# Kernel optimization log

Hardware: AMD Instinct MI355X
Metric: run time of the kernel (lower is better)

The kernel has to match this reference:

```python
import jax, jax.numpy as jnp
import numpy as np

STEP = 1  # spatial shift amount (module hard-codes narrow offset 1, so step=1)
EPS = 1e-5  # BatchNorm eps (torch default)


def conv1x1(x, W, b):
    # x: [B,C,H,W], W: [Co,C], b: [Co]
    return jnp.einsum('bchw,oc->bohw', x, W) + b[None, :, None, None]


def setup_inputs() -> dict:
    key = jax.random.key(0)
    ks = jax.random.split(key, 16)
    B, C, H, W = 32, 160, 112, 112
    Co = C // 5
    d = {}
    d['x'] = jax.random.normal(ks[0], (B, C, H, W), dtype=jnp.float32)
    # BatchNorm (inference-style) params
    d['gamma'] = jax.random.uniform(ks[1], (C,), minval=0.8, maxval=1.2)
    d['beta'] = jax.random.normal(ks[2], (C,)) * 0.05
    d['running_mean'] = jax.random.normal(ks[3], (C,)) * 0.1
    d['running_var'] = jax.random.uniform(ks[4], (C,), minval=0.5, maxval=1.5)
    # five 1x1 branch convs: weight [Co, C], bias [Co]
    names = ['t', 'b', 'r', 'l', 'c']
    for i, n in enumerate(names):
        d[f'W_{n}'] = jax.random.normal(ks[5 + i], (Co, C)) * 0.05
        d[f'b_{n}'] = jnp.zeros((Co,), dtype=jnp.float32)
    # final fuse conv: [C, C]
    d['W_fuse'] = jax.random.normal(ks[10], (C, C)) * 0.05
    d['b_fuse'] = jnp.zeros((C,), dtype=jnp.float32)
    return d


def reference(x, gamma, beta, running_mean, running_var,
              W_t, b_t, W_b, b_b, W_r, b_r, W_l, b_l, W_c, b_c,
              W_fuse, b_fuse):
    B, C, H, Wd = x.shape
    # BatchNorm2d (inference) + exact GELU (torch default)
    inv = gamma / jnp.sqrt(running_var + EPS)
    h = (x - running_mean[None, :, None, None]) * inv[None, :, None, None] + beta[None, :, None, None]
    h = jax.nn.gelu(h, approximate=False)
    # five parallel 1x1 projections, each C -> C//5
    xt = conv1x1(h, W_t, b_t)
    xb = conv1x1(h, W_b, b_b)
    xr = conv1x1(h, W_r, b_r)
    xl = conv1x1(h, W_l, b_l)
    xc = conv1x1(h, W_c, b_c)
    # spatial shifts: pad + narrow (torch F.pad order is (left,right,top,bottom))
    # x_t: pad bottom by STEP, take rows [1, 1+H)  -> shift up
    xt = jnp.pad(xt, ((0, 0), (0, 0), (0, STEP), (0, 0)))[:, :, 1:1 + H, :]
    # x_b: pad top by STEP, take rows [0, H)       -> shift down
    xb = jnp.pad(xb, ((0, 0), (0, 0), (STEP, 0), (0, 0)))[:, :, :H, :]
    # x_l: pad right by STEP, take cols [1, 1+W)   -> shift left
    xl = jnp.pad(xl, ((0, 0), (0, 0), (0, 0), (0, STEP)))[:, :, :, 1:1 + Wd]
    # x_r: pad left by STEP, take cols [0, W)      -> shift right
    xr = jnp.pad(xr, ((0, 0), (0, 0), (0, 0), (STEP, 0)))[:, :, :, :Wd]
    # concat in original order [t, b, r, l, c] then final 1x1 fuse
    cat = jnp.concatenate([xt, xb, xr, xl, xc], axis=1)  # [B, C, H, W]
    return conv1x1(cat, W_fuse, b_fuse)
```

## Files before the change

### kernel.cpp

```cpp
#include <hip/hip_runtime.h>
#include <hip/hip_bf16.h>

#define BATCH 32
#define C 160
#define H 112
#define W 112
#define HW (H * W)
#define NT 7

typedef __bf16 bf16_t;
typedef bf16_t bf16x8 __attribute__((ext_vector_type(8)));
typedef float f32x4 __attribute__((ext_vector_type(4)));

#define P_BYTES   ((size_t)BATCH * C * HW * 2)
#define WALL_OFF  (P_BYTES)
#define WFRAG_B   (10 * 5 * 64 * 8 * 2)
#define WFUSE_OFF (WALL_OFF + WFRAG_B)
#define BN2_OFF   (WFUSE_OFF + WFRAG_B)
#define BALL_OFF  (BN2_OFF + C * 8)

__global__ __launch_bounds__(256) void prep_kernel(
    const float* __restrict__ Wt, const float* __restrict__ Wb,
    const float* __restrict__ Wr, const float* __restrict__ Wl,
    const float* __restrict__ Wc,
    const float* __restrict__ bt, const float* __restrict__ bb,
    const float* __restrict__ br, const float* __restrict__ bl,
    const float* __restrict__ bc,
    const float* __restrict__ Wfuse,
    const float* __restrict__ gamma, const float* __restrict__ beta,
    const float* __restrict__ mean, const float* __restrict__ var,
    char* __restrict__ ws)
{
    bf16_t* wallf  = (bf16_t*)(ws + WALL_OFF);
    bf16_t* wfusef = (bf16_t*)(ws + WFUSE_OFF);
    float2* bn2 = (float2*)(ws + BN2_OFF);
    float*  ball = (float*)(ws + BALL_OFF);

    const float* Wbr[5] = {Wt, Wb, Wr, Wl, Wc};
    const float* bbr[5] = {bt, bb, br, bl, bc};

    int tid = blockIdx.x * blockDim.x + threadIdx.x;
    int nth = gridDim.x * blockDim.x;

    for (int idx = tid; idx < 10 * 5 * 64 * 8; idx += nth) {
        int j    = idx & 7;
        int lane = (idx >> 3) & 63;
        int rest = idx >> 9;
        int ks   = rest % 5;
        int mt   = rest / 5;
        int m  = mt * 16 + (lane & 15);
        int q  = lane >> 4;
        int k_nat = ks * 32 + q * 8 + j;
        wallf[idx] = (bf16_t)Wbr[m >> 5][(m & 31) * C + k_nat];
        int chan32 = (j < 4) ? (q * 4 + j) : (16 + q * 4 + (j - 4));
        wfusef[idx] = (bf16_t)Wfuse[m * C + ks * 32 + chan32];
    }
    for (int c = tid; c < C; c += nth) {
        float s = gamma[c] * rsqrtf(var[c] + 1e-5f);
        bn2[c] = make_float2(s, beta[c] - mean[c] * s);
        ball[c] = bbr[c >> 5][c & 31];
    }
}

__global__ __launch_bounds__(256) void stage1_kernel(
    const float* __restrict__ x, char* __restrict__ ws)
{
    const bf16_t* __restrict__ wallf = (const bf16_t*)(ws + WALL_OFF);
    const float2* __restrict__ bn2 = (const float2*)(ws + BN2_OFF);
    const float*  __restrict__ ball = (const float*)(ws + BALL_OFF);
    bf16_t* __restrict__ P = (bf16_t*)ws;

    int wid  = blockIdx.x * 4 + (threadIdx.x >> 6);
    int lane = threadIdx.x & 63;
    int b   = wid / (NT * H);
    int rem = wid - b * (NT * H);
    int y   = rem / NT;
    int t   = rem - y * NT;
    int nl = lane & 15, quad = lane >> 4;
    int px = t * 16 + nl;

    const float* xp = x + (size_t)b * C * HW + (size_t)y * W + px;

    float v[40];
#pragma unroll
    for (int i = 0; i < 40; ++i) {
        int ks = i >> 3, j = i & 7;
        v[i] = xp[(size_t)(ks * 32 + quad * 8 + j) * HW];
    }

    f32x4 acc[10];
#pragma unroll
    for (int mt = 0; mt < 10; ++mt)
        acc[mt] = *(const f32x4*)&ball[mt * 16 + quad * 4];

#pragma unroll
    for (int ks = 0; ks < 5; ++ks) {
        bf16x8 bfrag;
#pragma unroll
        for (int j = 0; j < 8; ++j) {
            int c = ks * 32 + quad * 8 + j;
            float2 sb = bn2[c];
            float h = v[ks * 8 + j] * sb.x + sb.y;
            float u  = h * 0.70710678118654752f;
            float au = __builtin_fabsf(u);
            float tt = __builtin_amdgcn_rcpf(__builtin_fmaf(0.3275911f, au, 1.0f));
            float poly = tt * __builtin_fmaf(tt,
                              __builtin_fmaf(tt,
                              __builtin_fmaf(tt,
                              __builtin_fmaf(tt, 1.061405429f, -1.453152027f),
                                                 1.421413741f),
                                                -0.284496736f),
                                                 0.254829592f);
            float e  = __builtin_amdgcn_exp2f(-au * au * 1.4426950408889634f);
            float er = __builtin_fmaf(-poly, e, 1.0f);
            er = __builtin_copysignf(er, u);
            h = 0.5f * h * (1.0f + er);
            bfrag[j] = (bf16_t)h;
        }
#pragma unroll
        for (int mt = 0; mt < 10; ++mt) {
            bf16x8 afrag = *(const bf16x8*)&wallf[((mt * 5 + ks) * 64 + lane) * 8];
            acc[mt] = __builtin_amdgcn_mfma_f32_16x16x32_bf16(afrag, bfrag, acc[mt], 0, 0, 0);
        }
    }

    size_t pb = (((size_t)(b * 5) * H + y) * W + px) * 32 + quad * 8;
#pragma unroll
    for (int kb = 0; kb < 5; ++kb) {
        bf16x8 o;
#pragma unroll
        for (int r = 0; r < 4; ++r) {
            o[r]     = (bf16_t)acc[kb * 2][r];
            o[r + 4] = (bf16_t)acc[kb * 2 + 1][r];
        }
        *(bf16x8*)&P[pb + (size_t)kb * HW * 32] = o;
    }
}

__global__ __launch_bounds__(256) void stage2_kernel(
    char* __restrict__ ws, const float* __restrict__ bfuse,
    float* __restrict__ out)
{
    const bf16_t* __restrict__ wfusef = (const bf16_t*)(ws + WFUSE_OFF);
    const bf16_t* __restrict__ P = (const bf16_t*)ws;

    int wid  = blockIdx.x * 4 + (threadIdx.x >> 6);
    int lane = threadIdx.x & 63;
    int b   = wid / (NT * H);
    int rem = wid - b * (NT * H);
    int y   = rem / NT;
    int t   = rem - y * NT;
    int nl = lane & 15, quad = lane >> 4;
    int px = t * 16 + nl;

    f32x4 acc[10];
#pragma unroll
    for (int mt = 0; mt < 10; ++mt)
        acc[mt] = *(const f32x4*)&bfuse[mt * 16 + quad * 4];

    bf16x8 zero;
#pragma unroll
    for (int j = 0; j < 8; ++j) zero[j] = (bf16_t)0.0f;

    auto ldP = [&](int kb, int yy, int xx) -> bf16x8 {
        return *(const bf16x8*)&P[(((size_t)(b * 5 + kb) * H + yy) * W + xx) * 32 + quad * 8];
    };

    bf16x8 f[5];
    f[0] = ldP(0, y + 1, px); if (y + 1 >= H) f[0] = zero;
    f[1] = ldP(1, y - 1, px); if (y == 0)     f[1] = zero;
    f[2] = ldP(2, y, px - 1); if (px == 0)    f[2] = zero;
    f[3] = ldP(3, y, px + 1); if (px == W - 1) f[3] = zero;
    f[4] = ldP(4, y, px);

#pragma unroll
    for (int ks = 0; ks < 5; ++ks) {
#pragma unroll
        for (int mt = 0; mt < 10; ++mt) {
            bf16x8 afrag = *(const bf16x8*)&wfusef[((mt * 5 + ks) * 64 + lane) * 8];
            acc[mt] = __builtin_amdgcn_mfma_f32_16x16x32_bf16(afrag, f[ks], acc[mt], 0, 0, 0);
        }
    }

    size_t ob = (size_t)b * C * HW + (size_t)y * W + px;
#pragma unroll
    for (int mt = 0; mt < 10; ++mt) {
#pragma unroll
        for (int r = 0; r < 4; ++r) {
            int m = mt * 16 + quad * 4 + r;
            out[ob + (size_t)m * HW] = acc[mt][r];
        }
    }
}

extern "C" void kernel_launch(void* const* d_in, const int* in_sizes, int n_in,
                              void* d_out, int out_size, void* d_ws, size_t ws_size,
                              hipStream_t stream)
{
    const float* x     = (const float*)d_in[0];
    const float* gamma = (const float*)d_in[1];
    const float* beta  = (const float*)d_in[2];
    const float* mean  = (const float*)d_in[3];
    const float* var   = (const float*)d_in[4];
    const float* Wt    = (const float*)d_in[5];
    const float* bt    = (const float*)d_in[6];
    const float* Wb    = (const float*)d_in[7];
    const float* bb    = (const float*)d_in[8];
    const float* Wr    = (const float*)d_in[9];
    const float* br    = (const float*)d_in[10];
    const float* Wl    = (const float*)d_in[11];
    const float* bl    = (const float*)d_in[12];
    const float* Wc    = (const float*)d_in[13];
    const float* bc    = (const float*)d_in[14];
    const float* Wfuse = (const float*)d_in[15];
    const float* bfuse = (const float*)d_in[16];

    char* ws = (char*)d_ws;
    float* out = (float*)d_out;

    prep_kernel<<<64, 256, 0, stream>>>(Wt, Wb, Wr, Wl, Wc, bt, bb, br, bl, bc,
                                        Wfuse, gamma, beta, mean, var, ws);

    int nblocks = (BATCH * H * NT) / 4;
    stage1_kernel<<<nblocks, 256, 0, stream>>>(x, ws);
    stage2_kernel<<<nblocks, 256, 0, stream>>>(ws, bfuse, out);
}
```

Baseline: 606.3 us.

## Process two rows per wave to reuse weight fragments and batch loads

Each wave in both stages now handles two adjacent image rows instead of one. Every weight fragment load is shared by two MFMAs, and all global loads are issued up front behind a sched_barrier to raise memory-level parallelism. Stage2 clamps its shifted addresses and zeroes them after the loads rather than before. The cost is roughly double the register pressure (80 input floats and 20 accumulators); launch_bounds(256,2) is added, which may limit occupancy or cause spills.

```diff
diff --git a/kernel.cpp b/kernel.cpp
--- a/kernel.cpp
+++ b/kernel.cpp
@@ -7,6 +7,7 @@
 #define W 112
 #define HW (H * W)
 #define NT 7
+#define HP (H / 2)
 
 typedef __bf16 bf16_t;
 typedef bf16_t bf16x8 __attribute__((ext_vector_type(8)));
@@ -18,6 +19,23 @@
 #define WFUSE_OFF (WALL_OFF + WFRAG_B)
 #define BN2_OFF   (WFUSE_OFF + WFRAG_B)
 #define BALL_OFF  (BN2_OFF + C * 8)
+
+__device__ __forceinline__ float gelu_exact(float h) {
+    float u  = h * 0.70710678118654752f;
+    float au = __builtin_fabsf(u);
+    float tt = __builtin_amdgcn_rcpf(__builtin_fmaf(0.3275911f, au, 1.0f));
+    float poly = tt * __builtin_fmaf(tt,
+                      __builtin_fmaf(tt,
+                      __builtin_fmaf(tt,
+                      __builtin_fmaf(tt, 1.061405429f, -1.453152027f),
+                                         1.421413741f),
+                                        -0.284496736f),
+                                         0.254829592f);
+    float e  = __builtin_amdgcn_exp2f(-au * au * 1.4426950408889634f);
+    float er = __builtin_fmaf(-poly, e, 1.0f);
+    er = __builtin_copysignf(er, u);
+    return 0.5f * h * (1.0f + er);
+}
 
 __global__ __launch_bounds__(256) void prep_kernel(
     const float* __restrict__ Wt, const float* __restrict__ Wb,
@@ -62,7 +80,7 @@
     }
 }
 
-__global__ __launch_bounds__(256) void stage1_kernel(
+__global__ __launch_bounds__(256, 2) void stage1_kernel(
     const float* __restrict__ x, char* __restrict__ ws)
 {
     const bf16_t* __restrict__ wallf = (const bf16_t*)(ws + WALL_OFF);
@@ -72,72 +90,69 @@
 
     int wid  = blockIdx.x * 4 + (threadIdx.x >> 6);
     int lane = threadIdx.x & 63;
-    int b   = wid / (NT * H);
-    int rem = wid - b * (NT * H);
-    int y   = rem / NT;
-    int t   = rem - y * NT;
+    int b   = wid / (HP * NT);
+    int rem = wid - b * (HP * NT);
+    int yp  = rem / NT;
+    int t   = rem - yp * NT;
+    int y0  = yp * 2;
     int nl = lane & 15, quad = lane >> 4;
     int px = t * 16 + nl;
 
-    const float* xp = x + (size_t)b * C * HW + (size_t)y * W + px;
-
-    float v[40];
+    const float* xp = x + (size_t)b * C * HW + (size_t)y0 * W + px;
+
+    float v0[40], v1[40];
 #pragma unroll
     for (int i = 0; i < 40; ++i) {
         int ks = i >> 3, j = i & 7;
-        v[i] = xp[(size_t)(ks * 32 + quad * 8 + j) * HW];
-    }
-
-    f32x4 acc[10];
-#pragma unroll
-    for (int mt = 0; mt < 10; ++mt)
-        acc[mt] = *(const f32x4*)&ball[mt * 16 + quad * 4];
+        size_t off = (size_t)(ks * 32 + quad * 8 + j) * HW;
+        v0[i] = xp[off];
+        v1[i] = xp[off + W];
+    }
+    __builtin_amdgcn_sched_barrier(0);
+
+    f32x4 acc0[10], acc1[10];
+#pragma unroll
+    for (int mt = 0; mt < 10; ++mt) {
+        f32x4 bias = *(const f32x4*)&ball[mt * 16 + quad * 4];
+        acc0[mt] = bias;
+        acc1[mt] = bias;
+    }
 
 #pragma unroll
     for (int ks = 0; ks < 5; ++ks) {
-        bf16x8 bfrag;
+        bf16x8 bfrag0, bfrag1;
 #pragma unroll
         for (int j = 0; j < 8; ++j) {
             int c = ks * 32 + quad * 8 + j;
             float2 sb = bn2[c];
-            float h = v[ks * 8 + j] * sb.x + sb.y;
-            float u  = h * 0.70710678118654752f;
-            float au = __builtin_fabsf(u);
-            float tt = __builtin_amdgcn_rcpf(__builtin_fmaf(0.3275911f, au, 1.0f));
-            float poly = tt * __builtin_fmaf(tt,
-                              __builtin_fmaf(tt,
-                              __builtin_fmaf(tt,
-                              __builtin_fmaf(tt, 1.061405429f, -1.453152027f),
-                                                 1.421413741f),
-                                                -0.284496736f),
-                                                 0.254829592f);
-            float e  = __builtin_amdgcn_exp2f(-au * au * 1.4426950408889634f);
-            float er = __builtin_fmaf(-poly, e, 1.0f);
-            er = __builtin_copysignf(er, u);
-            h = 0.5f * h * (1.0f + er);
-            bfrag[j] = (bf16_t)h;
+            bfrag0[j] = (bf16_t)gelu_exact(__builtin_fmaf(v0[ks * 8 + j], sb.x, sb.y));
+            bfrag1[j] = (bf16_t)gelu_exact(__builtin_fmaf(v1[ks * 8 + j], sb.x, sb.y));
         }
 #pragma unroll
         for (int mt = 0; mt < 10; ++mt) {
             bf16x8 afrag = *(const bf16x8*)&wallf[((mt * 5 + ks) * 64 + lane) * 8];
-            acc[mt] = __builtin_amdgcn_mfma_f32_16x16x32_bf16(afrag, bfrag, acc[mt], 0, 0, 0);
-        }
-    }
-
-    size_t pb = (((size_t)(b * 5) * H + y) * W + px) * 32 + quad * 8;
+            acc0[mt] = __builtin_amdgcn_mfma_f32_16x16x32_bf16(afrag, bfrag0, acc0[mt], 0, 0, 0);
+            acc1[mt] = __builtin_amdgcn_mfma_f32_16x16x32_bf16(afrag, bfrag1, acc1[mt], 0, 0, 0);
+        }
+    }
+
+    size_t pb = (((size_t)(b * 5) * H + y0) * W + px) * 32 + quad * 8;
 #pragma unroll
     for (int kb = 0; kb < 5; ++kb) {
-        bf16x8 o;
+        bf16x8 o0, o1;
 #pragma unroll
         for (int r = 0; r < 4; ++r) {
-            o[r]     = (bf16_t)acc[kb * 2][r];
-            o[r + 4] = (bf16_t)acc[kb * 2 + 1][r];
-        }
-        *(bf16x8*)&P[pb + (size_t)kb * HW * 32] = o;
-    }
-}
-
-__global__ __launch_bounds__(256) void stage2_kernel(
+            o0[r]     = (bf16_t)acc0[kb * 2][r];
+            o0[r + 4] = (bf16_t)acc0[kb * 2 + 1][r];
+            o1[r]     = (bf16_t)acc1[kb * 2][r];
+            o1[r + 4] = (bf16_t)acc1[kb * 2 + 1][r];
+        }
+        *(bf16x8*)&P[pb + (size_t)kb * HW * 32] = o0;
+        *(bf16x8*)&P[pb + (size_t)kb * HW * 32 + (size_t)W * 32] = o1;
+    }
+}
+
+__global__ __launch_bounds__(256, 2) void stage2_kernel(
     char* __restrict__ ws, const float* __restrict__ bfuse,
     float* __restrict__ out)
 {
@@ -146,17 +161,13 @@
 
     int wid  = blockIdx.x * 4 + (threadIdx.x >> 6);
     int lane = threadIdx.x & 63;
-    int b   = wid / (NT * H);
-    int rem = wid - b * (NT * H);
-    int y   = rem / NT;
-    int t   = rem - y * NT;
+    int b   = wid / (HP * NT);
+    int rem = wid - b * (HP * NT);
+    int yp  = rem / NT;
+    int t   = rem - yp * NT;
+    int y0  = yp * 2, y1 = y0 + 1;
     int nl = lane & 15, quad = lane >> 4;
     int px = t * 16 + nl;
-
-    f32x4 acc[10];
-#pragma unroll
-    for (int mt = 0; mt < 10; ++mt)
-        acc[mt] = *(const f32x4*)&bfuse[mt * 16 + quad * 4];
 
     bf16x8 zero;
 #pragma unroll
@@ -166,29 +177,50 @@
         return *(const bf16x8*)&P[(((size_t)(b * 5 + kb) * H + yy) * W + xx) * 32 + quad * 8];
     };
 
-    bf16x8 f[5];
-    f[0] = ldP(0, y + 1, px); if (y + 1 >= H) f[0] = zero;
-    f[1] = ldP(1, y - 1, px); if (y == 0)     f[1] = zero;
-    f[2] = ldP(2, y, px - 1); if (px == 0)    f[2] = zero;
-    f[3] = ldP(3, y, px + 1); if (px == W - 1) f[3] = zero;
-    f[4] = ldP(4, y, px);
+    bf16x8 f0[5], f1[5];
+    f0[0] = ldP(0, y0 + 1, px);
+    f0[1] = ldP(1, y0 - 1 < 0 ? 0 : y0 - 1, px);
+    f0[2] = ldP(2, y0, px == 0 ? 0 : px - 1);
+    f0[3] = ldP(3, y0, px == W - 1 ? px : px + 1);
+    f0[4] = ldP(4, y0, px);
+    f1[0] = ldP(0, y1 + 1 >= H ? y1 : y1 + 1, px);
+    f1[1] = ldP(1, y1 - 1, px);
+    f1[2] = ldP(2, y1, px == 0 ? 0 : px - 1);
+    f1[3] = ldP(3, y1, px == W - 1 ? px : px + 1);
+    f1[4] = ldP(4, y1, px);
+    __builtin_amdgcn_sched_barrier(0);
+
+    if (y0 == 0)     f0[1] = zero;
+    if (y1 + 1 >= H) f1[0] = zero;
+    if (px == 0)     { f0[2] = zero; f1[2] = zero; }
+    if (px == W - 1) { f0[3] = zero; f1[3] = zero; }
+
+    f32x4 acc0[10], acc1[10];
+#pragma unroll
+    for (int mt = 0; mt < 10; ++mt) {
+        f32x4 bias = *(const f32x4*)&bfuse[mt * 16 + quad * 4];
+        acc0[mt] = bias;
+        acc1[mt] = bias;
+    }
 
 #pragma unroll
     for (int ks = 0; ks < 5; ++ks) {
 #pragma unroll
         for (int mt = 0; mt < 10; ++mt) {
             bf16x8 afrag = *(const bf16x8*)&wfusef[((mt * 5 + ks) * 64 + lane) * 8];
-            acc[mt] = __builtin_amdgcn_mfma_f32_16x16x32_bf16(afrag, f[ks], acc[mt], 0, 0, 0);
-        }
-    }
-
-    size_t ob = (size_t)b * C * HW + (size_t)y * W + px;
+            acc0[mt] = __builtin_amdgcn_mfma_f32_16x16x32_bf16(afrag, f0[ks], acc0[mt], 0, 0, 0);
+            acc1[mt] = __builtin_amdgcn_mfma_f32_16x16x32_bf16(afrag, f1[ks], acc1[mt], 0, 0, 0);
+        }
+    }
+
+    size_t ob = (size_t)b * C * HW + (size_t)y0 * W + px;
 #pragma unroll
     for (int mt = 0; mt < 10; ++mt) {
 #pragma unroll
         for (int r = 0; r < 4; ++r) {
             int m = mt * 16 + quad * 4 + r;
-            out[ob + (size_t)m * HW] = acc[mt][r];
+            out[ob + (size_t)m * HW] = acc0[mt][r];
+            out[ob + (size_t)m * HW + W] = acc1[mt][r];
         }
     }
 }
@@ -221,7 +253,7 @@
     prep_kernel<<<64, 256, 0, stream>>>(Wt, Wb, Wr, Wl, Wc, bt, bb, br, bl, bc,
                                         Wfuse, gamma, beta, mean, var, ws);
 
-    int nblocks = (BATCH * H * NT) / 4;
+    int nblocks = (BATCH * HP * NT) / 4;
     stage1_kernel<<<nblocks, 256, 0, stream>>>(x, ws);
     stage2_kernel<<<nblocks, 256, 0, stream>>>(ws, bfuse, out);
 }
```

After: 590.1 us. -2.7%, faster.
